# Kernel tuning notes

Hardware: AMD Instinct MI355X
Metric: run time of the kernel (lower is better)

The kernel has to match this reference:

```python
import jax, jax.numpy as jnp
import numpy as np
from jax import lax

DN = ('NHWC', 'HWIO', 'NHWC')
F = 16  # ConvLSTM2D filters


def hard_sigmoid(x):
    return jnp.clip(x * 0.2 + 0.5, 0.0, 1.0)


def setup_inputs() -> dict:
    key = jax.random.key(0)
    ks = jax.random.split(key, 6)
    B, T, H, W, C = 8, 16, 640, 480, 1
    inputs = jax.random.normal(ks[0], (B, T, H, W, C), dtype=jnp.float32)
    # ConvLSTM2D params: kernel (3,3,Cin,4F) for gates i,f,c,o; recurrent kernel (3,3,F,4F)
    kernel = jax.random.normal(ks[1], (3, 3, C, 4 * F), dtype=jnp.float32) * 0.1
    rec_kernel = jax.random.normal(ks[2], (3, 3, F, 4 * F), dtype=jnp.float32) * 0.1
    bias = jnp.zeros((4 * F,), dtype=jnp.float32).at[F:2 * F].set(1.0)  # unit_forget_bias
    flat_dim = 318 * 238 * F  # valid 3x3 conv on 320x240
    dense_w = jax.random.normal(ks[3], (flat_dim, 1), dtype=jnp.float32) * (1.0 / np.sqrt(flat_dim))
    dense_b = jnp.zeros((1,), dtype=jnp.float32)
    return {"inputs": inputs, "kernel": kernel, "rec_kernel": rec_kernel,
            "bias": bias, "dense_w": dense_w, "dense_b": dense_b}


def _forward(inputs, kernel, rec_kernel, bias, dense_w, dense_b):
    # MaxPooling3D pool_size=(1,2,2), stride=(1,2,2), valid padding
    x = lax.reduce_window(inputs, -jnp.inf, lax.max,
                          (1, 1, 2, 2, 1), (1, 1, 2, 2, 1), 'VALID')
    B, T, H, W, C = x.shape
    # Input-to-gate convs are time-invariant: batch them over B*T (valid padding)
    xconv = lax.conv_general_dilated(x.reshape(B * T, H, W, C), kernel,
                                     (1, 1), 'VALID', dimension_numbers=DN) + bias
    Hc, Wc = xconv.shape[1], xconv.shape[2]
    xconv = xconv.reshape(B, T, Hc, Wc, 4 * F).transpose(1, 0, 2, 3, 4)  # (T,B,Hc,Wc,4F)

    h0 = jnp.zeros((B, Hc, Wc, F), dtype=x.dtype)
    c0 = jnp.zeros((B, Hc, Wc, F), dtype=x.dtype)

    def step(carry, xc):
        h, c = carry
        # recurrent conv always uses 'same' padding in Keras ConvLSTM2D
        z = xc + lax.conv_general_dilated(h, rec_kernel, (1, 1), 'SAME',
                                          dimension_numbers=DN)
        zi, zf, zc, zo = jnp.split(z, 4, axis=-1)  # gate order i, f, c, o
        i = hard_sigmoid(zi)
        f = hard_sigmoid(zf)
        c_new = f * c + i * jnp.tanh(zc)
        h_new = hard_sigmoid(zo) * jnp.tanh(c_new)
        return (h_new, c_new), None

    (h, _), _ = lax.scan(step, (h0, c0), xconv)
    flat = h.reshape(B, -1)
    return flat @ dense_w + dense_b  # (B, 1)


def reference(inputs, kernel, rec_kernel, bias, dense_w, dense_b):
    return _forward(inputs, kernel, rec_kernel, bias, dense_w, dense_b)
```

## Files before the change

kernel.cpp:

```cpp
#include <hip/hip_runtime.h>
#include <hip/hip_bf16.h>
#include <cstdint>

#define B_  8
#define T_  16
#define HIN 640
#define WIN 480
#define HP  320
#define WP  240
#define HO  318
#define WO  238

typedef unsigned short u16;
typedef unsigned int   u32;
typedef __attribute__((ext_vector_type(8))) short bf16x8;
typedef __attribute__((ext_vector_type(4))) float f32x4;

#define TY    4
#define PITCH 16
#define NFRAG 25
#define NBY   80
#define NWG   (4 * NBY * B_)

__device__ __forceinline__ u16 f2bf(float f) {
    u32 u = __float_as_uint(f);
    return (u16)((u + 0x7fffu + ((u >> 16) & 1u)) >> 16);
}
__device__ __forceinline__ float bf2f(u16 u) {
    return __uint_as_float(((u32)u) << 16);
}
__device__ __forceinline__ float h2f(u16 u) {
    _Float16 h = __builtin_bit_cast(_Float16, u);
    return (float)h;
}
__device__ __forceinline__ u16 f2h(float f) {
    _Float16 h = (_Float16)f;
    return __builtin_bit_cast(u16, h);
}
__device__ __forceinline__ float hsg(float v) {
    return __builtin_amdgcn_fmed3f(fmaf(v, 0.2f, 0.5f), 0.0f, 1.0f);
}
__device__ __forceinline__ float tanh_fast(float x) {
    float e = __expf(2.0f * x);
    return 1.0f - __fdividef(2.0f, e + 1.0f);
}

__global__ void pool_kernel(const float* __restrict__ in, u32* __restrict__ out) {
    int idx = blockIdx.x * 256 + threadIdx.x;
    const int total = B_ * T_ * HP * (WP / 2);
    if (idx >= total) return;
    int xp   = idx % (WP / 2);
    int rest = idx / (WP / 2);
    int y    = rest % HP;
    int bt   = rest / HP;
    const float* src = in + ((size_t)bt * HIN + 2 * y) * WIN + xp * 4;
    float4 a = *(const float4*)src;
    float4 b = *(const float4*)(src + WIN);
    float m0 = fmaxf(fmaxf(a.x, a.y), fmaxf(b.x, b.y));
    float m1 = fmaxf(fmaxf(a.z, a.w), fmaxf(b.z, b.w));
    out[((size_t)bt * HP + y) * (WP / 2) + xp] = (u32)f2bf(m0) | ((u32)f2bf(m1) << 16);
}

__global__ void frag_build(const float* __restrict__ krec, const float* __restrict__ kin,
                           int4* __restrict__ fragbuf) {
    int idx = blockIdx.x * 256 + threadIdx.x;
    if (idx >= NFRAG * 64) return;
    int l = idx & 63, f = idx >> 6;
    int lo = (f >= 20);
    int q  = lo ? (f - 20) : (f >> 2);
    int nt = lo ? 2 : (f & 3);
    int n = nt * 16 + (l & 15), o = l >> 4;
    u16 u[8];
    #pragma unroll
    for (int j = 0; j < 8; ++j) {
        int k = q * 32 + o * 8 + j;
        float wv = 0.0f;
        if (k < 144) wv = krec[k * 64 + n];
        else if (k < 153) wv = kin[(k - 144) * 64 + n];
        u16 hi = f2bf(wv);
        u[j] = lo ? f2bf(wv - bf2f(hi)) : hi;
    }
    int4 v;
    v.x = (int)((u32)u[0] | ((u32)u[1] << 16));
    v.y = (int)((u32)u[2] | ((u32)u[3] << 16));
    v.z = (int)((u32)u[4] | ((u32)u[5] << 16));
    v.w = (int)((u32)u[6] | ((u32)u[7] << 16));
    fragbuf[f * 64 + l] = v;
}

__global__ __launch_bounds__(256, 4)
void lstm_step(const u16* __restrict__ xpb, int t,
               const u16* __restrict__ hin,
               u16* __restrict__ hout,
               u16* __restrict__ cbuf,
               const int4* __restrict__ fragbuf,
               const float* __restrict__ bias, int lastT) {
    __shared__ __align__(16) u16 sh_h[6 * 66 * PITCH];
    __shared__ __align__(16) u16 sxf[2 * 256 * 8];

    const int tid  = threadIdx.x;
    const int wgid = blockIdx.x;
    const int b    = wgid & 7;
    const int by   = wgid >> 5;
    const int bx   = (wgid >> 3) & 3;
    const int newid = b * 320 + by * 4 + bx;
    const int wv_ = tid >> 6;
    const int l   = tid & 63;
    const int y0  = by * TY;
    const int x0  = bx * 64;
    const int o   = l >> 4;
    const int ch  = l & 15;
    const bool fast = (t > 0) & (x0 >= 1) & (x0 <= 173) & (y0 >= 1) & (y0 <= 313);

    if (fast) {
        const u16* hb = hin + (((size_t)b * HO + y0 - 1) * WO + x0 - 1) * 16;
        #pragma unroll
        for (int k = 0; k < 4; ++k) {
            const int unit = k * 256 + tid;
            if (unit < 792) {
                const int px = unit >> 1, half = unit & 1;
                const int hr = px / 66, hx = px - hr * 66;
                const u16* g = hb + ((size_t)hr * WO + hx) * 16 + half * 8;
                u16* lp = sh_h + (size_t)(k * 256 + wv_ * 64) * 8;
                __builtin_amdgcn_global_load_lds(
                    (const __attribute__((address_space(1))) void*)g,
                    (__attribute__((address_space(3))) void*)lp, 16, 0, 0);
            }
        }
    } else {
        for (int i = tid; i < 6 * 66; i += 256) {
            int hr = i / 66, hx = i - hr * 66;
            int gy = y0 - 1 + hr, gx = x0 - 1 + hx;
            bool ok = (t > 0) && gy >= 0 && gy < HO && gx >= 0 && gx < WO;
            int4 v0 = make_int4(0, 0, 0, 0), v1 = v0;
            if (ok) {
                const int4* g = (const int4*)&hin[(((size_t)b * HO + gy) * WO + gx) * 16];
                v0 = g[0]; v1 = g[1];
            }
            u16* d = &sh_h[i * PITCH];
            *(int4*)d = v0; *(int4*)(d + 8) = v1;
        }
    }

    int4 c01 = make_int4(0, 0, 0, 0), c23 = c01;
    if (t > 0) {
        const int4* cp = (const int4*)cbuf + ((size_t)newid * 256 + tid) * 2;
        c01 = cp[0]; c23 = cp[1];
    }

    {
        const int sxi = tid & 63, m = tid >> 6;
        const u16* xs = xpb + (size_t)(b * T_ + t) * HP * WP;
        u16 u[9];
        if (fast) {
            const u16* xr = xs + (size_t)(y0 + m) * WP + x0 + sxi;
            #pragma unroll
            for (int j = 0; j < 9; ++j) u[j] = xr[(j / 3) * WP + (j % 3)];
        } else {
            #pragma unroll
            for (int j = 0; j < 9; ++j) {
                int gy = y0 + m + j / 3, gx = x0 + sxi + j % 3;
                u[j] = (gy < HP && gx < WP) ? xs[(size_t)gy * WP + gx] : (u16)0;
            }
        }
        int4 p;
        p.x = (int)((u32)u[0] | ((u32)u[1] << 16));
        p.y = (int)((u32)u[2] | ((u32)u[3] << 16));
        p.z = (int)((u32)u[4] | ((u32)u[5] << 16));
        p.w = (int)((u32)u[6] | ((u32)u[7] << 16));
        *(int4*)&sxf[tid * 8] = p;
        *(int4*)&sxf[(256 + tid) * 8] = make_int4((int)(u32)u[8], 0, 0, 0);
    }
    __syncthreads();

    float bv[4];
    #pragma unroll
    for (int nt = 0; nt < 4; ++nt) bv[nt] = bias[nt * 16 + ch];

    f32x4 acc[TY][4];
    #pragma unroll
    for (int m = 0; m < TY; ++m)
        #pragma unroll
        for (int nt = 0; nt < 4; ++nt)
            acc[m][nt] = (f32x4){bv[nt], bv[nt], bv[nt], bv[nt]};

    const int ci0  = (o & 1) * 8;
    const bool hiH = (l >= 32);
    const int wx   = wv_ * 16 + (l & 15);
    const int4* fbl = fragbuf + l;

    int4 nb0 = fbl[0 * 64], nb1 = fbl[1 * 64], nb2 = fbl[2 * 64], nb3 = fbl[3 * 64];
    #pragma unroll 1
    for (int q = 0; q < 4; ++q) {
        bf16x8 Bh0 = __builtin_bit_cast(bf16x8, nb0);
        bf16x8 Bh1 = __builtin_bit_cast(bf16x8, nb1);
        bf16x8 Bh2 = __builtin_bit_cast(bf16x8, nb2);
        bf16x8 Bh3 = __builtin_bit_cast(bf16x8, nb3);
        nb0 = fbl[((q + 1) * 4 + 0) * 64];
        nb1 = fbl[((q + 1) * 4 + 1) * 64];
        nb2 = fbl[((q + 1) * 4 + 2) * 64];
        nb3 = fbl[((q + 1) * 4 + 3) * 64];
        const int tap = 2 * q + (hiH ? 1 : 0);
        const int dy = tap / 3, dx = tap - 3 * dy;
        #pragma unroll
        for (int m = 0; m < TY; ++m) {
            bf16x8 Ah = *(const bf16x8*)&sh_h[((m + dy) * 66 + wx + dx) * PITCH + ci0];
            acc[m][0] = __builtin_amdgcn_mfma_f32_16x16x32_bf16(Ah, Bh0, acc[m][0], 0, 0, 0);
            acc[m][1] = __builtin_amdgcn_mfma_f32_16x16x32_bf16(Ah, Bh1, acc[m][1], 0, 0, 0);
            acc[m][2] = __builtin_amdgcn_mfma_f32_16x16x32_bf16(Ah, Bh2, acc[m][2], 0, 0, 0);
            acc[m][3] = __builtin_amdgcn_mfma_f32_16x16x32_bf16(Ah, Bh3, acc[m][3], 0, 0, 0);
        }
    }
    {
        bf16x8 Bh0 = __builtin_bit_cast(bf16x8, nb0);
        bf16x8 Bh1 = __builtin_bit_cast(bf16x8, nb1);
        bf16x8 Bh2 = __builtin_bit_cast(bf16x8, nb2);
        bf16x8 Bh3 = __builtin_bit_cast(bf16x8, nb3);
        #pragma unroll
        for (int m = 0; m < TY; ++m) {
            bf16x8 Ah;
            if (!hiH) {
                Ah = *(const bf16x8*)&sh_h[((m + 2) * 66 + wx + 2) * PITCH + ci0];
            } else {
                const int slot = (o == 2 ? 0 : 256) + m * 64 + wx;
                Ah = *(const bf16x8*)&sxf[slot * 8];
            }
            acc[m][0] = __builtin_amdgcn_mfma_f32_16x16x32_bf16(Ah, Bh0, acc[m][0], 0, 0, 0);
            acc[m][1] = __builtin_amdgcn_mfma_f32_16x16x32_bf16(Ah, Bh1, acc[m][1], 0, 0, 0);
            acc[m][2] = __builtin_amdgcn_mfma_f32_16x16x32_bf16(Ah, Bh2, acc[m][2], 0, 0, 0);
            acc[m][3] = __builtin_amdgcn_mfma_f32_16x16x32_bf16(Ah, Bh3, acc[m][3], 0, 0, 0);
        }
    }

    u16 cl[16];
    {
        u32 d;
        d = (u32)c01.x; cl[0] = (u16)d;  cl[1] = (u16)(d >> 16);
        d = (u32)c01.y; cl[2] = (u16)d;  cl[3] = (u16)(d >> 16);
        d = (u32)c01.z; cl[4] = (u16)d;  cl[5] = (u16)(d >> 16);
        d = (u32)c01.w; cl[6] = (u16)d;  cl[7] = (u16)(d >> 16);
        d = (u32)c23.x; cl[8] = (u16)d;  cl[9] = (u16)(d >> 16);
        d = (u32)c23.y; cl[10] = (u16)d; cl[11] = (u16)(d >> 16);
        d = (u32)c23.z; cl[12] = (u16)d; cl[13] = (u16)(d >> 16);
        d = (u32)c23.w; cl[14] = (u16)d; cl[15] = (u16)(d >> 16);
    }
    u16 cs[16];

    if (fast) {
        #pragma unroll
        for (int m = 0; m < TY; ++m) {
            size_t rowb = (((size_t)b * HO + y0 + m) * WO + x0 + wv_ * 16 + o * 4) * 16 + ch;
            #pragma unroll
            for (int r = 0; r < 4; ++r) {
                float co = h2f(cl[m * 4 + r]);
                float zi = acc[m][0][r], zf = acc[m][1][r], zc = acc[m][2][r], zo = acc[m][3][r];
                float cn = fmaf(hsg(zf), co, hsg(zi) * tanh_fast(zc));
                float hn = hsg(zo) * tanh_fast(cn);
                cs[m * 4 + r] = f2h(cn);
                hout[rowb + (size_t)r * 16] = f2bf(hn);
            }
        }
    } else {
        #pragma unroll
        for (int m = 0; m < TY; ++m) {
            const int y = y0 + m;
            #pragma unroll
            for (int r = 0; r < 4; ++r) {
                const int x = x0 + wv_ * 16 + o * 4 + r;
                float co = h2f(cl[m * 4 + r]);
                float zi = acc[m][0][r], zf = acc[m][1][r], zc = acc[m][2][r], zo = acc[m][3][r];
                float cn = fmaf(hsg(zf), co, hsg(zi) * tanh_fast(zc));
                float hn = hsg(zo) * tanh_fast(cn);
                cs[m * 4 + r] = f2h(cn);
                if (y < HO && x < WO)
                    hout[(((size_t)b * HO + y) * WO + x) * 16 + ch] = f2bf(hn);
            }
        }
    }
    if (!lastT) {
        int4 o01, o23;
        o01.x = (int)((u32)cs[0]  | ((u32)cs[1]  << 16));
        o01.y = (int)((u32)cs[2]  | ((u32)cs[3]  << 16));
        o01.z = (int)((u32)cs[4]  | ((u32)cs[5]  << 16));
        o01.w = (int)((u32)cs[6]  | ((u32)cs[7]  << 16));
        o23.x = (int)((u32)cs[8]  | ((u32)cs[9]  << 16));
        o23.y = (int)((u32)cs[10] | ((u32)cs[11] << 16));
        o23.z = (int)((u32)cs[12] | ((u32)cs[13] << 16));
        o23.w = (int)((u32)cs[14] | ((u32)cs[15] << 16));
        int4* cp = (int4*)cbuf + ((size_t)newid * 256 + tid) * 2;
        cp[0] = o01; cp[1] = o23;
    }
}

#define NPX    (HO * WO)
#define PCHUNK 512
#define NCHUNK ((NPX + PCHUNK - 1) / PCHUNK)

__device__ __forceinline__ float dot2(u32 a, float w0, float w1, float s) {
    s = fmaf(bf2f((u16)a), w0, s);
    return fmaf(bf2f((u16)(a >> 16)), w1, s);
}

__global__ void dense1(const u16* __restrict__ h, const float* __restrict__ w,
                       float* __restrict__ partial) {
    int b = blockIdx.y, tid = threadIdx.x;
    const u16* hb = h + (size_t)b * NPX * 16;
    float s = 0.0f;
    #pragma unroll
    for (int pp = 0; pp < 2; ++pp) {
        int px = blockIdx.x * PCHUNK + tid * 2 + pp;
        if (px < NPX) {
            const int4* g = (const int4*)&hb[(size_t)px * 16];
            int4 a0 = g[0], a1 = g[1];
            const float4* wp = (const float4*)&w[(size_t)px * 16];
            float4 w0 = wp[0], w1 = wp[1], w2 = wp[2], w3 = wp[3];
            s = dot2((u32)a0.x, w0.x, w0.y, s);
            s = dot2((u32)a0.y, w0.z, w0.w, s);
            s = dot2((u32)a0.z, w1.x, w1.y, s);
            s = dot2((u32)a0.w, w1.z, w1.w, s);
            s = dot2((u32)a1.x, w2.x, w2.y, s);
            s = dot2((u32)a1.y, w2.z, w2.w, s);
            s = dot2((u32)a1.z, w3.x, w3.y, s);
            s = dot2((u32)a1.w, w3.z, w3.w, s);
        }
    }
    #pragma unroll
    for (int of = 32; of > 0; of >>= 1) s += __shfl_down(s, of, 64);
    __shared__ float red[4];
    if ((tid & 63) == 0) red[tid >> 6] = s;
    __syncthreads();
    if (tid == 0) partial[b * NCHUNK + blockIdx.x] = red[0] + red[1] + red[2] + red[3];
}

__global__ void dense2(const float* __restrict__ partial, const float* __restrict__ db,
                       float* __restrict__ out) {
    int b = blockIdx.x, tid = threadIdx.x;
    float s = 0.0f;
    for (int i = tid; i < NCHUNK; i += 256) s += partial[b * NCHUNK + i];
    #pragma unroll
    for (int of = 32; of > 0; of >>= 1) s += __shfl_down(s, of, 64);
    __shared__ float red[4];
    if ((tid & 63) == 0) red[tid >> 6] = s;
    __syncthreads();
    if (tid == 0) out[b] = red[0] + red[1] + red[2] + red[3] + db[0];
}

extern "C" void kernel_launch(void* const* d_in, const int* in_sizes, int n_in,
                              void* d_out, int out_size, void* d_ws, size_t ws_size,
                              hipStream_t stream) {
    const float* inputs = (const float*)d_in[0];
    const float* kin    = (const float*)d_in[1];
    const float* krec   = (const float*)d_in[2];
    const float* bias   = (const float*)d_in[3];
    const float* dw     = (const float*)d_in[4];
    const float* db     = (const float*)d_in[5];
    float* out = (float*)d_out;

    const size_t XPN = (size_t)B_ * T_ * HP * WP;
    const size_t HN  = (size_t)B_ * HO * WO * 16;
    const size_t CN  = (size_t)NWG * 256 * 16;

    u16*   xp   = (u16*)d_ws;
    u16*   h0   = xp + XPN;
    u16*   h1   = h0 + HN;
    u16*   cbuf = h1 + HN;
    int4*  frag = (int4*)(cbuf + CN);
    float* part = (float*)(frag + NFRAG * 64);

    {
        int total = B_ * T_ * HP * (WP / 2);
        pool_kernel<<<(total + 255) / 256, 256, 0, stream>>>(inputs, (u32*)xp);
    }
    frag_build<<<(NFRAG * 64 + 255) / 256, 256, 0, stream>>>(krec, kin, frag);

    for (int t = 0; t < T_; ++t) {
        const u16* hi = (t & 1) ? h1 : h0;
        u16*       ho = (t & 1) ? h0 : h1;
        lstm_step<<<NWG, 256, 0, stream>>>(xp, t, hi, ho, cbuf, frag, bias, (t == T_ - 1));
    }
    dense1<<<dim3(NCHUNK, B_), 256, 0, stream>>>(h0, dw, part);
    dense2<<<B_, 256, 0, stream>>>(part, db, out);
}
```

Baseline: 521.0 us.

## Fuse max-pooling into the per-timestep LSTM kernel, drop pooled buffer

Removes the separate pooling kernel and the bf16 pooled-input buffer. Each LSTM step now reads the raw fp32 input tile with a halo, does the 2x2 max-pool, and stages the result in shared memory, adding one extra barrier. The 3x3 input patch is then gathered from shared memory instead of scattered global loads. This saves one kernel launch and the write plus reread of the pooled tensor, at the cost of reading about four times more raw data per step, with some halo reads repeated. The c-state index also changes from the remapped newid to wgid, which is a consistent store and load layout.

```diff
diff --git a/kernel.cpp b/kernel.cpp
--- a/kernel.cpp
+++ b/kernel.cpp
@@ -43,22 +43,6 @@
 __device__ __forceinline__ float tanh_fast(float x) {
     float e = __expf(2.0f * x);
     return 1.0f - __fdividef(2.0f, e + 1.0f);
-}
-
-__global__ void pool_kernel(const float* __restrict__ in, u32* __restrict__ out) {
-    int idx = blockIdx.x * 256 + threadIdx.x;
-    const int total = B_ * T_ * HP * (WP / 2);
-    if (idx >= total) return;
-    int xp   = idx % (WP / 2);
-    int rest = idx / (WP / 2);
-    int y    = rest % HP;
-    int bt   = rest / HP;
-    const float* src = in + ((size_t)bt * HIN + 2 * y) * WIN + xp * 4;
-    float4 a = *(const float4*)src;
-    float4 b = *(const float4*)(src + WIN);
-    float m0 = fmaxf(fmaxf(a.x, a.y), fmaxf(b.x, b.y));
-    float m1 = fmaxf(fmaxf(a.z, a.w), fmaxf(b.z, b.w));
-    out[((size_t)bt * HP + y) * (WP / 2) + xp] = (u32)f2bf(m0) | ((u32)f2bf(m1) << 16);
 }
 
 __global__ void frag_build(const float* __restrict__ krec, const float* __restrict__ kin,
@@ -89,7 +73,7 @@
 }
 
 __global__ __launch_bounds__(256, 4)
-void lstm_step(const u16* __restrict__ xpb, int t,
+void lstm_step(const float* __restrict__ inp, int t,
                const u16* __restrict__ hin,
                u16* __restrict__ hout,
                u16* __restrict__ cbuf,
@@ -97,20 +81,21 @@
                const float* __restrict__ bias, int lastT) {
     __shared__ __align__(16) u16 sh_h[6 * 66 * PITCH];
     __shared__ __align__(16) u16 sxf[2 * 256 * 8];
+    __shared__ u16 sh_x[6 * 66];
 
     const int tid  = threadIdx.x;
     const int wgid = blockIdx.x;
     const int b    = wgid & 7;
     const int by   = wgid >> 5;
     const int bx   = (wgid >> 3) & 3;
-    const int newid = b * 320 + by * 4 + bx;
     const int wv_ = tid >> 6;
     const int l   = tid & 63;
     const int y0  = by * TY;
     const int x0  = bx * 64;
     const int o   = l >> 4;
     const int ch  = l & 15;
-    const bool fast = (t > 0) & (x0 >= 1) & (x0 <= 173) & (y0 >= 1) & (y0 <= 313);
+    const bool fast  = (t > 0) & (x0 >= 1) & (x0 <= 173) & (y0 >= 1) & (y0 <= 313);
+    const bool pfast = (x0 != 192) & (y0 <= 312);
 
     if (fast) {
         const u16* hb = hin + (((size_t)b * HO + y0 - 1) * WO + x0 - 1) * 16;
@@ -144,25 +129,43 @@
 
     int4 c01 = make_int4(0, 0, 0, 0), c23 = c01;
     if (t > 0) {
-        const int4* cp = (const int4*)cbuf + ((size_t)newid * 256 + tid) * 2;
+        const int4* cp = (const int4*)cbuf + ((size_t)wgid * 256 + tid) * 2;
         c01 = cp[0]; c23 = cp[1];
     }
+
+    {
+        const float* xs = inp + (size_t)(b * T_ + t) * HIN * WIN;
+        if (pfast) {
+            for (int i = tid; i < 6 * 66; i += 256) {
+                int row = i / 66, col = i - row * 66;
+                const float* p0 = xs + ((size_t)(2 * (y0 + row)) * WIN + 2 * (x0 + col));
+                float2 a  = *(const float2*)p0;
+                float2 b2 = *(const float2*)(p0 + WIN);
+                sh_x[i] = f2bf(fmaxf(fmaxf(a.x, a.y), fmaxf(b2.x, b2.y)));
+            }
+        } else {
+            for (int i = tid; i < 6 * 66; i += 256) {
+                int row = i / 66, col = i - row * 66;
+                int gy = y0 + row, gx = x0 + col;
+                u16 v = 0;
+                if (gy < HP && gx < WP) {
+                    const float* p0 = xs + ((size_t)(2 * gy) * WIN + 2 * gx);
+                    float2 a  = *(const float2*)p0;
+                    float2 b2 = *(const float2*)(p0 + WIN);
+                    v = f2bf(fmaxf(fmaxf(a.x, a.y), fmaxf(b2.x, b2.y)));
+                }
+                sh_x[i] = v;
+            }
+        }
+    }
+    __syncthreads();
 
     {
         const int sxi = tid & 63, m = tid >> 6;
-        const u16* xs = xpb + (size_t)(b * T_ + t) * HP * WP;
         u16 u[9];
-        if (fast) {
-            const u16* xr = xs + (size_t)(y0 + m) * WP + x0 + sxi;
-            #pragma unroll
-            for (int j = 0; j < 9; ++j) u[j] = xr[(j / 3) * WP + (j % 3)];
-        } else {
-            #pragma unroll
-            for (int j = 0; j < 9; ++j) {
-                int gy = y0 + m + j / 3, gx = x0 + sxi + j % 3;
-                u[j] = (gy < HP && gx < WP) ? xs[(size_t)gy * WP + gx] : (u16)0;
-            }
-        }
+        #pragma unroll
+        for (int j = 0; j < 9; ++j)
+            u[j] = sh_x[(m + j / 3) * 66 + sxi + (j % 3)];
         int4 p;
         p.x = (int)((u32)u[0] | ((u32)u[1] << 16));
         p.y = (int)((u32)u[2] | ((u32)u[3] << 16));
@@ -287,7 +290,7 @@
         o23.y = (int)((u32)cs[10] | ((u32)cs[11] << 16));
         o23.z = (int)((u32)cs[12] | ((u32)cs[13] << 16));
         o23.w = (int)((u32)cs[14] | ((u32)cs[15] << 16));
-        int4* cp = (int4*)cbuf + ((size_t)newid * 256 + tid) * 2;
+        int4* cp = (int4*)cbuf + ((size_t)wgid * 256 + tid) * 2;
         cp[0] = o01; cp[1] = o23;
     }
 }
@@ -356,27 +359,21 @@
     const float* db     = (const float*)d_in[5];
     float* out = (float*)d_out;
 
-    const size_t XPN = (size_t)B_ * T_ * HP * WP;
-    const size_t HN  = (size_t)B_ * HO * WO * 16;
-    const size_t CN  = (size_t)NWG * 256 * 16;
-
-    u16*   xp   = (u16*)d_ws;
-    u16*   h0   = xp + XPN;
+    const size_t HN = (size_t)B_ * HO * WO * 16;
+    const size_t CN = (size_t)NWG * 256 * 16;
+
+    u16*   h0   = (u16*)d_ws;
     u16*   h1   = h0 + HN;
     u16*   cbuf = h1 + HN;
     int4*  frag = (int4*)(cbuf + CN);
     float* part = (float*)(frag + NFRAG * 64);
 
-    {
-        int total = B_ * T_ * HP * (WP / 2);
-        pool_kernel<<<(total + 255) / 256, 256, 0, stream>>>(inputs, (u32*)xp);
-    }
     frag_build<<<(NFRAG * 64 + 255) / 256, 256, 0, stream>>>(krec, kin, frag);
 
     for (int t = 0; t < T_; ++t) {
         const u16* hi = (t & 1) ? h1 : h0;
         u16*       ho = (t & 1) ? h0 : h1;
-        lstm_step<<<NWG, 256, 0, stream>>>(xp, t, hi, ho, cbuf, frag, bias, (t == T_ - 1));
+        lstm_step<<<NWG, 256, 0, stream>>>(inputs, t, hi, ho, cbuf, frag, bias, (t == T_ - 1));
     }
     dense1<<<dim3(NCHUNK, B_), 256, 0, stream>>>(h0, dw, part);
     dense2<<<B_, 256, 0, stream>>>(part, db, out);
```

After: 524.1 us. About the same (+0.6%).

## Fuse dense dot product into final LSTM step and drop dense1 kernel

Applied to the files above, without the earlier changes.

On the last timestep, the LSTM step kernel now multiplies each new h value by its dense weight and reduces the products per workgroup into a partial sum, instead of writing h to global memory. A separate dense kernel then no longer has to re-read h. The cell-state buffer is also indexed directly by workgroup id instead of a remapped id, which changes its access pattern. The cost of this is an extra weight load and a block reduction in the last step, plus a dense2 kernel that reads the partials with a stride of 8.

```diff
diff --git a/kernel.cpp b/kernel.cpp
--- a/kernel.cpp
+++ b/kernel.cpp
@@ -21,6 +21,7 @@
 #define NFRAG 25
 #define NBY   80
 #define NWG   (4 * NBY * B_)
+#define NPX   (HO * WO)
 
 __device__ __forceinline__ u16 f2bf(float f) {
     u32 u = __float_as_uint(f);
@@ -94,16 +95,19 @@
                u16* __restrict__ hout,
                u16* __restrict__ cbuf,
                const int4* __restrict__ fragbuf,
-               const float* __restrict__ bias, int lastT) {
+               const float* __restrict__ bias,
+               const float* __restrict__ dw,
+               float* __restrict__ part,
+               int lastT) {
     __shared__ __align__(16) u16 sh_h[6 * 66 * PITCH];
     __shared__ __align__(16) u16 sxf[2 * 256 * 8];
+    __shared__ float red[4];
 
     const int tid  = threadIdx.x;
     const int wgid = blockIdx.x;
     const int b    = wgid & 7;
     const int by   = wgid >> 5;
     const int bx   = (wgid >> 3) & 3;
-    const int newid = b * 320 + by * 4 + bx;
     const int wv_ = tid >> 6;
     const int l   = tid & 63;
     const int y0  = by * TY;
@@ -144,7 +148,7 @@
 
     int4 c01 = make_int4(0, 0, 0, 0), c23 = c01;
     if (t > 0) {
-        const int4* cp = (const int4*)cbuf + ((size_t)newid * 256 + tid) * 2;
+        const int4* cp = (const int4*)cbuf + ((size_t)wgid * 256 + tid) * 2;
         c01 = cp[0]; c23 = cp[1];
     }
 
@@ -245,6 +249,8 @@
         d = (u32)c23.w; cl[14] = (u16)d; cl[15] = (u16)(d >> 16);
     }
     u16 cs[16];
+    float dsum = 0.0f;
+    const size_t bbase = (size_t)b * NPX * 16;
 
     if (fast) {
         #pragma unroll
@@ -252,12 +258,14 @@
             size_t rowb = (((size_t)b * HO + y0 + m) * WO + x0 + wv_ * 16 + o * 4) * 16 + ch;
             #pragma unroll
             for (int r = 0; r < 4; ++r) {
+                size_t gc = rowb + (size_t)r * 16;
                 float co = h2f(cl[m * 4 + r]);
                 float zi = acc[m][0][r], zf = acc[m][1][r], zc = acc[m][2][r], zo = acc[m][3][r];
                 float cn = fmaf(hsg(zf), co, hsg(zi) * tanh_fast(zc));
                 float hn = hsg(zo) * tanh_fast(cn);
                 cs[m * 4 + r] = f2h(cn);
-                hout[rowb + (size_t)r * 16] = f2bf(hn);
+                if (!lastT) hout[gc] = f2bf(hn);
+                else        dsum = fmaf(bf2f(f2bf(hn)), dw[gc - bbase], dsum);
             }
         }
     } else {
@@ -272,8 +280,11 @@
                 float cn = fmaf(hsg(zf), co, hsg(zi) * tanh_fast(zc));
                 float hn = hsg(zo) * tanh_fast(cn);
                 cs[m * 4 + r] = f2h(cn);
-                if (y < HO && x < WO)
-                    hout[(((size_t)b * HO + y) * WO + x) * 16 + ch] = f2bf(hn);
+                if (y < HO && x < WO) {
+                    size_t gc = (((size_t)b * HO + y) * WO + x) * 16 + ch;
+                    if (!lastT) hout[gc] = f2bf(hn);
+                    else        dsum = fmaf(bf2f(f2bf(hn)), dw[gc - bbase], dsum);
+                }
             }
         }
     }
@@ -287,56 +298,22 @@
         o23.y = (int)((u32)cs[10] | ((u32)cs[11] << 16));
         o23.z = (int)((u32)cs[12] | ((u32)cs[13] << 16));
         o23.w = (int)((u32)cs[14] | ((u32)cs[15] << 16));
-        int4* cp = (int4*)cbuf + ((size_t)newid * 256 + tid) * 2;
+        int4* cp = (int4*)cbuf + ((size_t)wgid * 256 + tid) * 2;
         cp[0] = o01; cp[1] = o23;
-    }
-}
-
-#define NPX    (HO * WO)
-#define PCHUNK 512
-#define NCHUNK ((NPX + PCHUNK - 1) / PCHUNK)
-
-__device__ __forceinline__ float dot2(u32 a, float w0, float w1, float s) {
-    s = fmaf(bf2f((u16)a), w0, s);
-    return fmaf(bf2f((u16)(a >> 16)), w1, s);
-}
-
-__global__ void dense1(const u16* __restrict__ h, const float* __restrict__ w,
-                       float* __restrict__ partial) {
-    int b = blockIdx.y, tid = threadIdx.x;
-    const u16* hb = h + (size_t)b * NPX * 16;
-    float s = 0.0f;
-    #pragma unroll
-    for (int pp = 0; pp < 2; ++pp) {
-        int px = blockIdx.x * PCHUNK + tid * 2 + pp;
-        if (px < NPX) {
-            const int4* g = (const int4*)&hb[(size_t)px * 16];
-            int4 a0 = g[0], a1 = g[1];
-            const float4* wp = (const float4*)&w[(size_t)px * 16];
-            float4 w0 = wp[0], w1 = wp[1], w2 = wp[2], w3 = wp[3];
-            s = dot2((u32)a0.x, w0.x, w0.y, s);
-            s = dot2((u32)a0.y, w0.z, w0.w, s);
-            s = dot2((u32)a0.z, w1.x, w1.y, s);
-            s = dot2((u32)a0.w, w1.z, w1.w, s);
-            s = dot2((u32)a1.x, w2.x, w2.y, s);
-            s = dot2((u32)a1.y, w2.z, w2.w, s);
-            s = dot2((u32)a1.z, w3.x, w3.y, s);
-            s = dot2((u32)a1.w, w3.z, w3.w, s);
-        }
-    }
-    #pragma unroll
-    for (int of = 32; of > 0; of >>= 1) s += __shfl_down(s, of, 64);
-    __shared__ float red[4];
-    if ((tid & 63) == 0) red[tid >> 6] = s;
-    __syncthreads();
-    if (tid == 0) partial[b * NCHUNK + blockIdx.x] = red[0] + red[1] + red[2] + red[3];
-}
-
-__global__ void dense2(const float* __restrict__ partial, const float* __restrict__ db,
+    } else {
+        #pragma unroll
+        for (int of = 32; of > 0; of >>= 1) dsum += __shfl_down(dsum, of, 64);
+        if ((tid & 63) == 0) red[tid >> 6] = dsum;
+        __syncthreads();
+        if (tid == 0) part[wgid] = red[0] + red[1] + red[2] + red[3];
+    }
+}
+
+__global__ void dense2(const float* __restrict__ part, const float* __restrict__ db,
                        float* __restrict__ out) {
     int b = blockIdx.x, tid = threadIdx.x;
     float s = 0.0f;
-    for (int i = tid; i < NCHUNK; i += 256) s += partial[b * NCHUNK + i];
+    for (int k = tid; k < NBY * 4; k += 256) s += part[(size_t)k * 8 + b];
     #pragma unroll
     for (int of = 32; of > 0; of >>= 1) s += __shfl_down(s, of, 64);
     __shared__ float red[4];
@@ -376,8 +353,8 @@
     for (int t = 0; t < T_; ++t) {
         const u16* hi = (t & 1) ? h1 : h0;
         u16*       ho = (t & 1) ? h0 : h1;
-        lstm_step<<<NWG, 256, 0, stream>>>(xp, t, hi, ho, cbuf, frag, bias, (t == T_ - 1));
-    }
-    dense1<<<dim3(NCHUNK, B_), 256, 0, stream>>>(h0, dw, part);
+        lstm_step<<<NWG, 256, 0, stream>>>(xp, t, hi, ho, cbuf, frag, bias,
+                                           dw, part, (t == T_ - 1));
+    }
     dense2<<<B_, 256, 0, stream>>>(part, db, out);
 }
```

New measurement: 518.9 us. About the same (-0.4%).
